# Optimization experiments

Measured on AMD Instinct MI355X. Metric: run time of the kernel, lower is better.

The kernel has to match this reference:

```python
import jax, jax.numpy as jnp
import numpy as np

B, N, D_FEAT = 16, 4096, 64
NPOINT, NSAMPLE = 1024, 32
MLP = [64, 64, 128]
IN_CH = 3 + D_FEAT
EPS = 1e-5  # BatchNorm eps (torch default)


def _fps(xyz, npoint):
    # Farthest point sampling; sequential scan over npoint steps (matches torch loop).
    b, n, _ = xyz.shape
    def step(carry, _):
        distance, farthest = carry  # (B,N) running min dist, (B,) current centroid idx
        centroid = jnp.take_along_axis(xyz, farthest[:, None, None], axis=1)  # (B,1,3)
        d = jnp.sum((xyz - centroid) ** 2, -1)  # (B,N)
        distance = jnp.minimum(distance, d)
        nxt = jnp.argmax(distance, -1).astype(jnp.int32)
        return (distance, nxt), farthest
    init = (jnp.full((b, n), jnp.inf, dtype=xyz.dtype),
            jnp.full((b,), n // 2, dtype=jnp.int32))
    _, centroids = jax.lax.scan(step, init, None, length=npoint)
    return centroids.T  # (B, npoint)


def _gather(pts, idx):
    # pts: (B,N,C); idx: (B,...) int -> (B,...,C)
    return jax.vmap(lambda p, i: p[i])(pts, idx)


def setup_inputs() -> dict:
    key = jax.random.key(0)
    ks = jax.random.split(key, 16)
    inp = {
        'xyz': jax.random.normal(ks[0], (B, N, 3), jnp.float32),
        'points': jax.random.normal(ks[1], (B, N, D_FEAT), jnp.float32),
    }
    last = IN_CH
    for li, oc in enumerate(MLP):
        inp[f'W{li}'] = jax.random.normal(ks[2 + li], (oc, last), jnp.float32) * (1.0 / np.sqrt(last))
        inp[f'b{li}'] = jnp.zeros((oc,), jnp.float32)
        inp[f'g{li}'] = jnp.ones((oc,), jnp.float32)
        inp[f'be{li}'] = jnp.zeros((oc,), jnp.float32)
        last = oc
    C = MLP[-1]; R = C // 8
    inp['aW1'] = jax.random.normal(ks[10], (R, C), jnp.float32) * (1.0 / np.sqrt(C))
    inp['aW2'] = jax.random.normal(ks[11], (C, R), jnp.float32) * (1.0 / np.sqrt(R))
    return inp


def reference(xyz, points, W0, b0, g0, be0, W1, b1, g1, be1, W2, b2, g2, be2, aW1, aW2):
    fps_idx = _fps(xyz, NPOINT)                 # (B,S) int32
    new_xyz = _gather(xyz, fps_idx)             # (B,S,3)
    # squared distances (B,S,N) via matmul expansion (as torch square_distance)
    d = (-2.0 * jnp.einsum('bsc,bnc->bsn', new_xyz, xyz)
         + jnp.sum(new_xyz ** 2, -1)[..., None]
         + jnp.sum(xyz ** 2, -1)[:, None, :])
    _, idx = jax.lax.top_k(-d, NSAMPLE)         # (B,S,k) nearest neighbors
    grouped_xyz = _gather(xyz, idx)             # (B,S,k,3)
    rel = grouped_xyz - new_xyz[:, :, None, :]  # relative coords
    feat = _gather(points, idx)                 # (B,S,k,D)
    g = jnp.concatenate([rel, feat], axis=-1)   # (B,S,k,3+D) channels-last
    # 1x1 conv MLP + BatchNorm (training-mode batch stats) + ReLU
    for (W, b, ga, be) in ((W0, b0, g0, be0), (W1, b1, g1, be1), (W2, b2, g2, be2)):
        g = jnp.einsum('bskc,oc->bsko', g, W) + b
        mu = g.mean(axis=(0, 1, 2))
        var = g.var(axis=(0, 1, 2))
        g = ga * (g - mu) * jax.lax.rsqrt(var + EPS) + be
        g = jax.nn.relu(g)
    new_points = g.max(axis=2)                  # max over nsample -> (B,S,C)
    # channel attention on (B,C,S) == reductions over S here
    avg = new_points.mean(axis=1)               # (B,C)
    mx = new_points.max(axis=1)                 # (B,C)
    def fc(v):
        return jnp.einsum('cr,br->bc', aW2, jax.nn.relu(jnp.einsum('rc,bc->br', aW1, v)))
    scale = jax.nn.sigmoid(fc(avg) + fc(mx))    # (B,C)
    new_points = new_points * scale[:, None, :]
    return new_xyz, new_points, fps_idx
```

## Files before the change

kernel.cpp:

```cpp
#include <hip/hip_runtime.h>
#include <hip/hip_bf16.h>

#define BB 16
#define NN 4096
#define SS 1024
#define KS 32
#define DF 64
#define INC 67
#define C1 64
#define C2 64
#define C3 128
#define ROWS (BB*SS*KS)
#define EPSBN 1e-5f
#define F_INF (__builtin_inff())

typedef __bf16 bf16;
typedef __bf16 bfrag __attribute__((ext_vector_type(8)));
typedef float  ffrag __attribute__((ext_vector_type(4)));
typedef float  f2    __attribute__((ext_vector_type(2)));
typedef unsigned long long u64;

#define OUT_NXYZ 0
#define OUT_NP   49152
#define OUT_FPS  2146304

#define OFF_FPS   0u
#define OFF_NXYZ  65536u
#define OFF_IDX   262144u
#define OFF_STATS 2359296u
#define OFF_ASUM  2555904u
#define OFF_AMAX  2621440u
#define OFF_BNC   2686976u
#define OFF_SCALE 2690048u
#define OFF_NP0   2698240u
#define OFF_YMAX  11086848u
#define OFF_H1    19475456u
#define OFF_H2    86584320u
#define ZERO_BYTES (196608u + 65536u + 65536u)

#define DPP_MAX_STEP(k, ctrl, rmask, bc) { \
  int _lo = __builtin_amdgcn_update_dpp(0, (int)(unsigned)(k), (ctrl), (rmask), 0xf, (bc)); \
  int _hi = __builtin_amdgcn_update_dpp(0, (int)((k)>>32),     (ctrl), (rmask), 0xf, (bc)); \
  u64 _k2 = ((u64)(unsigned)_hi << 32) | (unsigned)_lo; \
  if (_k2 > (k)) (k) = _k2; }

#define DPP_FMAX_STEP(v, ctrl, rmask, bc) { \
  int _t = __builtin_amdgcn_update_dpp(0, __float_as_int(v), (ctrl), (rmask), 0xf, (bc)); \
  (v) = fmaxf((v), __uint_as_float((unsigned)_t)); }

__device__ __forceinline__ u64 dpp_wavemax64(u64 k){
  DPP_MAX_STEP(k, 0x111, 0xf, true)
  DPP_MAX_STEP(k, 0x112, 0xf, true)
  DPP_MAX_STEP(k, 0x114, 0xf, true)
  DPP_MAX_STEP(k, 0x118, 0xf, true)
  DPP_MAX_STEP(k, 0x142, 0xa, false)
  DPP_MAX_STEP(k, 0x143, 0xc, false)
  return k;
}

__device__ __forceinline__ u64 readlane64(u64 k, int lane){
  unsigned lo = (unsigned)__builtin_amdgcn_readlane((int)(unsigned)k, lane);
  unsigned hi = (unsigned)__builtin_amdgcn_readlane((int)(k >> 32),   lane);
  return ((u64)hi << 32) | lo;
}

__device__ __forceinline__ u64 umax64(u64 a, u64 b){ return a > b ? a : b; }

__global__ __launch_bounds__(256) void fps_kernel(const float* __restrict__ xyz,
                                                  int* __restrict__ fps_i,
                                                  float* __restrict__ nxyz_ws,
                                                  float* __restrict__ out)
{
  #pragma clang fp contract(off)
  __shared__ __align__(16) float4 lc[NN];
  __shared__ int lfps[SS];
  __shared__ __align__(16) u64 slotk[2][4];
  int b = blockIdx.x, t = threadIdx.x;
  const float* xb = xyz + (size_t)b*NN*3;
  for (int p = t; p < NN; p += 256){
    lc[p] = make_float4(xb[p*3], xb[p*3+1], xb[p*3+2], 0.f);
  }
  __syncthreads();
  f2 px2[8], py2[8], pz2[8], pd2[8];
  int p0 = t*16;
  #pragma unroll
  for (int j=0;j<8;++j){
    float4 a = lc[p0+2*j], c = lc[p0+2*j+1];
    px2[j] = (f2){a.x, c.x}; py2[j] = (f2){a.y, c.y}; pz2[j] = (f2){a.z, c.z};
    pd2[j] = (f2){F_INF, F_INF};
  }
  float cx = lc[NN/2].x, cy = lc[NN/2].y, cz = lc[NN/2].z;
  if (t==0) lfps[0]=NN/2;
  int wv = t >> 6, lane = t & 63;
  for (int it=1; it<SS; ++it){
    f2 c2x = (f2){cx,cx}, c2y = (f2){cy,cy}, c2z = (f2){cz,cz};
    float bvA=-1.f; int biA=p0;
    float bvB=-1.f; int biB=p0+8;
    #pragma unroll
    for (int j=0;j<4;++j){
      f2 dx = px2[j]-c2x, dy = py2[j]-c2y, dz = pz2[j]-c2z;
      f2 d = (dx*dx + dy*dy) + dz*dz;
      f2 nd = (f2){fminf(pd2[j].x, d.x), fminf(pd2[j].y, d.y)};
      pd2[j]=nd;
      if (nd.x > bvA){ bvA=nd.x; biA=p0+2*j; }
      if (nd.y > bvA){ bvA=nd.y; biA=p0+2*j+1; }
    }
    #pragma unroll
    for (int j=4;j<8;++j){
      f2 dx = px2[j]-c2x, dy = py2[j]-c2y, dz = pz2[j]-c2z;
      f2 d = (dx*dx + dy*dy) + dz*dz;
      f2 nd = (f2){fminf(pd2[j].x, d.x), fminf(pd2[j].y, d.y)};
      pd2[j]=nd;
      if (nd.x > bvB){ bvB=nd.x; biB=p0+2*j; }
      if (nd.y > bvB){ bvB=nd.y; biB=p0+2*j+1; }
    }
    float bv = bvA; int bi = biA;
    if (bvB > bvA){ bv = bvB; bi = biB; }
    float mv = bv;
    DPP_FMAX_STEP(mv, 0x111, 0xf, true)
    DPP_FMAX_STEP(mv, 0x112, 0xf, true)
    DPP_FMAX_STEP(mv, 0x114, 0xf, true)
    DPP_FMAX_STEP(mv, 0x118, 0xf, true)
    DPP_FMAX_STEP(mv, 0x142, 0xa, false)
    DPP_FMAX_STEP(mv, 0x143, 0xc, false)
    float wmax = __uint_as_float((unsigned)__builtin_amdgcn_readlane(__float_as_int(mv), 63));
    u64 em = __ballot(bv == wmax);
    int wl = (int)__builtin_ctzll(em);
    int wbi = __builtin_amdgcn_readlane(bi, wl);
    int p = it & 1;
    if (lane == 0)
      slotk[p][wv] = ((u64)__float_as_uint(wmax) << 32) | (unsigned)(~wbi);
    __syncthreads();
    ulonglong2 sA = *(const ulonglong2*)&slotk[p][0];
    ulonglong2 sB = *(const ulonglong2*)&slotk[p][2];
    u64 k = umax64(umax64(sA.x, sA.y), umax64(sB.x, sB.y));
    int i = ~(unsigned)k;
    float4 cc = lc[i];
    cx = cc.x; cy = cc.y; cz = cc.z;
    if (t==0) lfps[it]=i;
  }
  __syncthreads();
  for (int s=t; s<SS; s+=256){
    int i = lfps[s];
    fps_i[b*SS+s]=i;
    out[OUT_FPS + b*SS + s] = (float)i;
    float4 cc = lc[i];
    int o3 = (b*SS+s)*3;
    out[OUT_NXYZ+o3]=cc.x; out[OUT_NXYZ+o3+1]=cc.y; out[OUT_NXYZ+o3+2]=cc.z;
    nxyz_ws[o3]=cc.x; nxyz_ws[o3+1]=cc.y; nxyz_ws[o3+2]=cc.z;
  }
}

__global__ __launch_bounds__(64) void knn_kernel(const float* __restrict__ xyz,
                                                 const float* __restrict__ nxyz,
                                                 int* __restrict__ knn)
{
  __shared__ float ld[NN];
  int lane = threadIdx.x;
  int bs = blockIdx.x;
  int b = bs >> 10;
  const float* xb = xyz + (size_t)b*NN*3;
  float sx=nxyz[bs*3], sy=nxyz[bs*3+1], sz=nxyz[bs*3+2];
  float gv[8]; int gi[8];
  float lv = F_INF; int li = 0;
  #pragma unroll
  for (int g=0; g<8; ++g){
    float bgv = F_INF; int bgi = 0;
    #pragma unroll
    for (int jj=0; jj<8; ++jj){
      int p = (g*8+jj)*64 + lane;
      float dx=xb[p*3]-sx, dy=xb[p*3+1]-sy, dz=xb[p*3+2]-sz;
      float d = dx*dx+dy*dy+dz*dz;
      ld[p] = d;
      if (d < bgv){ bgv=d; bgi=p; }
    }
    gv[g]=bgv; gi[g]=bgi;
    if (bgv < lv){ lv=bgv; li=bgi; }
  }
  int kept = 0;
  for (int it=0; it<KS; ++it){
    u64 mk = ~(((u64)__float_as_uint(lv) << 32) | (unsigned)li);
    mk = dpp_wavemax64(mk);
    mk = readlane64(mk, 63);
    int i = (int)(unsigned)(~mk);
    if (lane==it) kept = i;
    if ((i & 63) == lane){
      int j = i >> 6;
      ld[i] = F_INF;
      int g = j >> 3;
      float bgv=F_INF; int bgi=0;
      for (int jj=0;jj<8;++jj){
        int p = (g*8+jj)*64 + lane;
        float d = ld[p];
        if (d<bgv){bgv=d;bgi=p;}
      }
      #pragma unroll
      for (int q=0;q<8;++q){ if (q==g){ gv[q]=bgv; gi[q]=bgi; } }
      lv=F_INF; li=0;
      #pragma unroll
      for (int q=0;q<8;++q){ if (gv[q]<lv){ lv=gv[q]; li=gi[q]; } }
    }
  }
  if (lane < KS) knn[bs*KS + lane] = kept;
}

__global__ __launch_bounds__(256) void conv1_kernel(const float* __restrict__ xyz,
                                                    const float* __restrict__ points,
                                                    const float* __restrict__ W0,
                                                    const float* __restrict__ b0,
                                                    const float* __restrict__ nxyz,
                                                    const int* __restrict__ knn,
                                                    bf16* __restrict__ h1,
                                                    float* __restrict__ stats)
{
  __shared__ __align__(16) bf16 As[64][104];
  __shared__ __align__(16) bf16 Bs[64][104];
  __shared__ float s1[C1], s2[C1];
  int t = threadIdx.x;
  int Rbase = blockIdx.x * 64;
  if (t < C1){ s1[t]=0.f; s2[t]=0.f; }
  {
    int o = t >> 2, q = t & 3;
    const float* wr = W0 + o*INC;
    for (int cc = q*24; cc < q*24+24; ++cc){
      float w;
      if (cc < 64) w = wr[3+cc];
      else if (cc < 67) w = wr[cc-64];
      else w = 0.f;
      Bs[o][cc] = (bf16)w;
    }
  }
  {
    int r = t >> 2, q = t & 3;
    int R = Rbase + r;
    int bs = R >> 5;
    int bIdx = bs >> 10;
    int nI = knn[R];
    const float* pr = points + ((size_t)(bIdx*NN + nI))*DF + q*16;
    float4 f0 = *(const float4*)(pr);
    float4 f1 = *(const float4*)(pr+4);
    float4 f2v = *(const float4*)(pr+8);
    float4 f3 = *(const float4*)(pr+12);
    bf16* ap = &As[r][q*16];
    ap[0]=(bf16)f0.x; ap[1]=(bf16)f0.y; ap[2]=(bf16)f0.z; ap[3]=(bf16)f0.w;
    ap[4]=(bf16)f1.x; ap[5]=(bf16)f1.y; ap[6]=(bf16)f1.z; ap[7]=(bf16)f1.w;
    ap[8]=(bf16)f2v.x; ap[9]=(bf16)f2v.y; ap[10]=(bf16)f2v.z; ap[11]=(bf16)f2v.w;
    ap[12]=(bf16)f3.x; ap[13]=(bf16)f3.y; ap[14]=(bf16)f3.z; ap[15]=(bf16)f3.w;
    if (q==0){
      const float* xr = xyz + ((size_t)(bIdx*NN + nI))*3;
      const float* nr = nxyz + bs*3;
      As[r][64]=(bf16)(xr[0]-nr[0]);
      As[r][65]=(bf16)(xr[1]-nr[1]);
      As[r][66]=(bf16)(xr[2]-nr[2]);
      for (int cc=67; cc<96; ++cc) As[r][cc]=(bf16)0.f;
    }
  }
  __syncthreads();
  int wv = t >> 6, lane = t & 63;
  int row16 = wv * 16;
  int arow = lane & 15, kgrp = lane >> 4;
  ffrag acc[4] = {};
  #pragma unroll
  for (int kc = 0; kc < 3; ++kc){
    bfrag af = *(const bfrag*)&As[row16 + arow][kc*32 + kgrp*8];
    #pragma unroll
    for (int nt = 0; nt < 4; ++nt){
      bfrag bfv = *(const bfrag*)&Bs[nt*16 + arow][kc*32 + kgrp*8];
      acc[nt] = __builtin_amdgcn_mfma_f32_16x16x32_bf16(af, bfv, acc[nt], 0,0,0);
    }
  }
  #pragma unroll
  for (int nt=0; nt<4; ++nt){
    int c = nt*16 + arow;
    float bias = b0[c];
    float ls1=0.f, ls2=0.f;
    #pragma unroll
    for (int r=0;r<4;++r){
      float y = acc[nt][r] + bias;
      int grow = Rbase + row16 + kgrp*4 + r;
      h1[(size_t)grow*C1 + c] = (bf16)y;
      ls1 += y; ls2 += y*y;
    }
    ls1 += __shfl_xor(ls1, 16); ls1 += __shfl_xor(ls1, 32);
    ls2 += __shfl_xor(ls2, 16); ls2 += __shfl_xor(ls2, 32);
    if (kgrp==0){ atomicAdd(&s1[c], ls1); atomicAdd(&s2[c], ls2); }
  }
  __syncthreads();
  if (t < C1){
    float* gp = stats + (blockIdx.x & 63)*256;
    atomicAdd(&gp[t], s1[t]);
    atomicAdd(&gp[128 + t], s2[t]);
  }
}

__global__ __launch_bounds__(256) void conv2_kernel(const bf16* __restrict__ h1,
                                                    const float* __restrict__ W1,
                                                    const float* __restrict__ b1,
                                                    const float* __restrict__ stats0,
                                                    const float* __restrict__ g0,
                                                    const float* __restrict__ be0,
                                                    bf16* __restrict__ h2,
                                                    float* __restrict__ stats)
{
  __shared__ __align__(16) bf16 As[64][72];
  __shared__ __align__(16) bf16 Bs[64][72];
  __shared__ float s1[C2], s2[C2];
  __shared__ float sbA[C2], sbB[C2];
  int t = threadIdx.x;
  int Rbase = blockIdx.x * 64;
  if (t < C2){ s1[t]=0.f; s2[t]=0.f; }
  if (t < C2){
    float a1=0.f, a2=0.f;
    for (int q=0;q<64;++q){ a1 += stats0[q*256+t]; a2 += stats0[q*256+128+t]; }
    float inv = 1.f/(float)ROWS;
    float mu = a1*inv; float var = a2*inv - mu*mu;
    float a = g0[t]*rsqrtf(var + EPSBN);
    sbA[t] = a; sbB[t] = be0[t] - mu*a;
  }
  {
    int o = t >> 2, q = t & 3;
    const float* wr = W1 + o*64 + q*16;
    bf16* bp = &Bs[o][q*16];
    #pragma unroll
    for (int v=0; v<4; ++v){
      float4 f = *(const float4*)(wr + v*4);
      bp[v*4+0]=(bf16)f.x; bp[v*4+1]=(bf16)f.y; bp[v*4+2]=(bf16)f.z; bp[v*4+3]=(bf16)f.w;
    }
  }
  __syncthreads();
  {
    int r = t >> 2, q = t & 3;
    int R = Rbase + r;
    const bf16* hr = h1 + (size_t)R*64 + q*16;
    bfrag h0 = *(const bfrag*)hr;
    bfrag h1v = *(const bfrag*)(hr+8);
    #pragma unroll
    for (int j=0;j<8;++j){
      int c=q*16+j;
      As[r][c] = (bf16)fmaxf(fmaf(sbA[c], (float)h0[j], sbB[c]), 0.f);
    }
    #pragma unroll
    for (int j=0;j<8;++j){
      int c=q*16+8+j;
      As[r][c] = (bf16)fmaxf(fmaf(sbA[c], (float)h1v[j], sbB[c]), 0.f);
    }
  }
  __syncthreads();
  int wv = t >> 6, lane = t & 63;
  int row16 = wv * 16;
  int arow = lane & 15, kgrp = lane >> 4;
  ffrag acc[4] = {};
  #pragma unroll
  for (int kc = 0; kc < 2; ++kc){
    bfrag af = *(const bfrag*)&As[row16 + arow][kc*32 + kgrp*8];
    #pragma unroll
    for (int nt = 0; nt < 4; ++nt){
      bfrag bfv = *(const bfrag*)&Bs[nt*16 + arow][kc*32 + kgrp*8];
      acc[nt] = __builtin_amdgcn_mfma_f32_16x16x32_bf16(af, bfv, acc[nt], 0,0,0);
    }
  }
  #pragma unroll
  for (int nt=0; nt<4; ++nt){
    int c = nt*16 + arow;
    float bias = b1[c];
    float ls1=0.f, ls2=0.f;
    #pragma unroll
    for (int r=0;r<4;++r){
      float y = acc[nt][r] + bias;
      int grow = Rbase + row16 + kgrp*4 + r;
      h2[(size_t)grow*C2 + c] = (bf16)y;
      ls1 += y; ls2 += y*y;
    }
    ls1 += __shfl_xor(ls1, 16); ls1 += __shfl_xor(ls1, 32);
    ls2 += __shfl_xor(ls2, 16); ls2 += __shfl_xor(ls2, 32);
    if (kgrp==0){ atomicAdd(&s1[c], ls1); atomicAdd(&s2[c], ls2); }
  }
  __syncthreads();
  if (t < C2){
    float* gp = stats + (blockIdx.x & 63)*256;
    atomicAdd(&gp[t], s1[t]);
    atomicAdd(&gp[128 + t], s2[t]);
  }
}

__global__ __launch_bounds__(256) void conv3_kernel(const bf16* __restrict__ h2,
                                                    const float* __restrict__ W2,
                                                    const float* __restrict__ b2,
                                                    const float* __restrict__ stats1,
                                                    const float* __restrict__ g1,
                                                    const float* __restrict__ be1,
                                                    float* __restrict__ ymax,
                                                    float* __restrict__ stats)
{
  __shared__ __align__(16) bf16 As[64][72];
  __shared__ __align__(16) bf16 Bs[128][72];
  __shared__ float s1[C3], s2[C3];
  __shared__ float wmax[4][C3];
  __shared__ float sbA[C2], sbB[C2];
  int t = threadIdx.x;
  int Rbase = blockIdx.x * 64;
  if (t < C3){ s1[t]=0.f; s2[t]=0.f; }
  if (t < C2){
    float a1=0.f, a2=0.f;
    for (int q=0;q<64;++q){ a1 += stats1[q*256+t]; a2 += stats1[q*256+128+t]; }
    float inv = 1.f/(float)ROWS;
    float mu = a1*inv; float var = a2*inv - mu*mu;
    float a = g1[t]*rsqrtf(var + EPSBN);
    sbA[t] = a; sbB[t] = be1[t] - mu*a;
  }
  {
    int o = t >> 1, q = t & 1;
    const float* wr = W2 + o*64 + q*32;
    bf16* bp = &Bs[o][q*32];
    #pragma unroll
    for (int v=0; v<8; ++v){
      float4 f = *(const float4*)(wr + v*4);
      bp[v*4+0]=(bf16)f.x; bp[v*4+1]=(bf16)f.y; bp[v*4+2]=(bf16)f.z; bp[v*4+3]=(bf16)f.w;
    }
  }
  __syncthreads();
  {
    int r = t >> 2, q = t & 3;
    int R = Rbase + r;
    const bf16* hr = h2 + (size_t)R*64 + q*16;
    bfrag h0 = *(const bfrag*)hr;
    bfrag h1v = *(const bfrag*)(hr+8);
    #pragma unroll
    for (int j=0;j<8;++j){
      int c=q*16+j;
      As[r][c] = (bf16)fmaxf(fmaf(sbA[c], (float)h0[j], sbB[c]), 0.f);
    }
    #pragma unroll
    for (int j=0;j<8;++j){
      int c=q*16+8+j;
      As[r][c] = (bf16)fmaxf(fmaf(sbA[c], (float)h1v[j], sbB[c]), 0.f);
    }
  }
  __syncthreads();
  int wv = t >> 6, lane = t & 63;
  int row16 = wv * 16;
  int arow = lane & 15, kgrp = lane >> 4;
  ffrag acc[8] = {};
  #pragma unroll
  for (int kc = 0; kc < 2; ++kc){
    bfrag af = *(const bfrag*)&As[row16 + arow][kc*32 + kgrp*8];
    #pragma unroll
    for (int nt = 0; nt < 8; ++nt){
      bfrag bfv = *(const bfrag*)&Bs[nt*16 + arow][kc*32 + kgrp*8];
      acc[nt] = __builtin_amdgcn_mfma_f32_16x16x32_bf16(af, bfv, acc[nt], 0,0,0);
    }
  }
  #pragma unroll
  for (int nt=0; nt<8; ++nt){
    int c = nt*16 + arow;
    float bias = b2[c];
    float ls1=0.f, ls2=0.f, mm=-F_INF;
    #pragma unroll
    for (int r=0;r<4;++r){
      float y = acc[nt][r] + bias;
      ls1 += y; ls2 += y*y; mm = fmaxf(mm, y);
    }
    ls1 += __shfl_xor(ls1, 16); ls1 += __shfl_xor(ls1, 32);
    ls2 += __shfl_xor(ls2, 16); ls2 += __shfl_xor(ls2, 32);
    mm = fmaxf(mm, __shfl_xor(mm, 16)); mm = fmaxf(mm, __shfl_xor(mm, 32));
    if (kgrp==0){ atomicAdd(&s1[c], ls1); atomicAdd(&s2[c], ls2); wmax[wv][c]=mm; }
  }
  __syncthreads();
  {
    int half = t >> 7;
    int c = t & 127;
    float m = fmaxf(wmax[half*2][c], wmax[half*2+1][c]);
    ymax[(size_t)(blockIdx.x*2 + half)*C3 + c] = m;
  }
  if (t < C3){
    float* gp = stats + (blockIdx.x & 63)*256;
    atomicAdd(&gp[t], s1[t]);
    atomicAdd(&gp[128 + t], s2[t]);
  }
}

__global__ __launch_bounds__(256) void attreduce_kernel(const float* __restrict__ ymax,
                                                        const float* __restrict__ stats2,
                                                        const float* __restrict__ g2,
                                                        const float* __restrict__ be2,
                                                        float* __restrict__ np0,
                                                        float* __restrict__ asum,
                                                        unsigned* __restrict__ amax)
{
  __shared__ float rs[256], rm[256];
  __shared__ float sbA[C3], sbB[C3];
  int t = threadIdx.x;
  if (t < C3){
    float a1=0.f, a2=0.f;
    for (int q=0;q<64;++q){ a1 += stats2[q*256+t]; a2 += stats2[q*256+128+t]; }
    float inv = 1.f/(float)ROWS;
    float mu = a1*inv; float var = a2*inv - mu*mu;
    float a = g2[t]*rsqrtf(var + EPSBN);
    sbA[t] = a; sbB[t] = be2[t] - mu*a;
  }
  __syncthreads();
  int b = blockIdx.x >> 3, sg = blockIdx.x & 7;
  int c = t & 127, h = t >> 7;
  float a = sbA[c], bb = sbB[c];
  size_t base = ((size_t)(b*1024 + sg*128 + h*64))*128 + c;
  float s = 0.f, m = 0.f;
  #pragma unroll 4
  for (int j=0;j<64;++j){
    float v = fmaxf(fmaf(a, ymax[base + (size_t)j*128], bb), 0.f);
    np0[base + (size_t)j*128] = v;
    s += v; m = fmaxf(m, v);
  }
  rs[t]=s; rm[t]=m;
  __syncthreads();
  if (t < 128){
    float s2 = rs[t] + rs[t+128];
    float m2 = fmaxf(rm[t], rm[t+128]);
    atomicAdd(&asum[b*128+t], s2);
    atomicMax(&amax[b*128+t], __float_as_uint(m2));
  }
}

__global__ __launch_bounds__(256) void attn_kernel(const float* __restrict__ asum,
                                                   const unsigned* __restrict__ amax,
                                                   const float* __restrict__ aW1,
                                                   const float* __restrict__ aW2,
                                                   float* __restrict__ scale)
{
  __shared__ float avg[16][128], mx[16][128], hA[16][16], hM[16][16];
  int t = threadIdx.x;
  for (int i=t; i<2048; i+=256){
    int b=i>>7, c=i&127;
    avg[b][c]=asum[i]*(1.f/1024.f); mx[b][c]=__uint_as_float(amax[i]);
  }
  __syncthreads();
  {
    int b=t>>4, r=t&15;
    float sa=0.f, sm=0.f;
    for (int c=0;c<128;++c){ float w=aW1[r*128+c]; sa+=w*avg[b][c]; sm+=w*mx[b][c]; }
    hA[b][r]=fmaxf(sa,0.f); hM[b][r]=fmaxf(sm,0.f);
  }
  __syncthreads();
  for (int i=t;i<2048;i+=256){
    int b=i>>7,c=i&127;
    float o=0.f;
    for (int r=0;r<16;++r){ o += aW2[c*16+r]*(hA[b][r]+hM[b][r]); }
    scale[i] = 1.f/(1.f+expf(-o));
  }
}

__global__ __launch_bounds__(256) void finout_kernel(const float* __restrict__ np0,
                                                     const float* __restrict__ scale,
                                                     float* __restrict__ out)
{
  int i = blockIdx.x*256 + threadIdx.x;
  int c = i & 127; int b = i >> 17;
  out[OUT_NP + i] = np0[i] * scale[b*128+c];
}

extern "C" void kernel_launch(void* const* d_in, const int* in_sizes, int n_in,
                              void* d_out, int out_size, void* d_ws, size_t ws_size,
                              hipStream_t stream)
{
  const float* xyz    = (const float*)d_in[0];
  const float* points = (const float*)d_in[1];
  const float* W0 = (const float*)d_in[2];
  const float* b0 = (const float*)d_in[3];
  const float* g0 = (const float*)d_in[4];
  const float* be0= (const float*)d_in[5];
  const float* W1 = (const float*)d_in[6];
  const float* b1 = (const float*)d_in[7];
  const float* g1 = (const float*)d_in[8];
  const float* be1= (const float*)d_in[9];
  const float* W2 = (const float*)d_in[10];
  const float* b2 = (const float*)d_in[11];
  const float* g2 = (const float*)d_in[12];
  const float* be2= (const float*)d_in[13];
  const float* aW1= (const float*)d_in[14];
  const float* aW2= (const float*)d_in[15];
  float* out = (float*)d_out;
  char* ws = (char*)d_ws;

  int*      fpsI  = (int*)(ws + OFF_FPS);
  float*    nxyz  = (float*)(ws + OFF_NXYZ);
  int*      knnI  = (int*)(ws + OFF_IDX);
  float*    stats = (float*)(ws + OFF_STATS);
  float*    asum  = (float*)(ws + OFF_ASUM);
  unsigned* amax  = (unsigned*)(ws + OFF_AMAX);
  float*    scl   = (float*)(ws + OFF_SCALE);
  float*    np0   = (float*)(ws + OFF_NP0);
  float*    ymax  = (float*)(ws + OFF_YMAX);
  bf16*     h1    = (bf16*)(ws + OFF_H1);
  bf16*     h2    = (bf16*)(ws + OFF_H2);

  hipMemsetAsync(ws + OFF_STATS, 0, ZERO_BYTES, stream);
  fps_kernel<<<BB, 256, 0, stream>>>(xyz, fpsI, nxyz, out);
  knn_kernel<<<BB*SS, 64, 0, stream>>>(xyz, nxyz, knnI);
  conv1_kernel<<<ROWS/64, 256, 0, stream>>>(xyz, points, W0, b0, nxyz, knnI, h1, stats);
  conv2_kernel<<<ROWS/64, 256, 0, stream>>>(h1, W1, b1, stats, g0, be0, h2, stats + 64*256);
  conv3_kernel<<<ROWS/64, 256, 0, stream>>>(h2, W2, b2, stats + 64*256, g1, be1, ymax, stats + 2*64*256);
  attreduce_kernel<<<BB*8, 256, 0, stream>>>(ymax, stats + 2*64*256, g2, be2, np0, asum, amax);
  attn_kernel<<<1, 256, 0, stream>>>(asum, amax, aW1, aW2, scl);
  finout_kernel<<<(BB*SS*C3)/256, 256, 0, stream>>>(np0, scl, out);
}
```

Baseline: 1.051 ms.

## Double conv row tiles to 128 rows per 512-thread block; merge FPS argmax chains

The three conv kernels now handle 128 rows per block with 512 threads. Each block loads and converts the weight tile once for twice as many rows and issues half as many stats atomics per row. In FPS, the two interleaved argmax chains become one sequential chain over all 8 pairs, which lowers register use but lengthens the dependency chain. Larger blocks also cut the number of blocks and may reduce occupancy. The serial FPS chain could be slower on what is likely the critical path.

```diff
diff --git a/kernel.cpp b/kernel.cpp
--- a/kernel.cpp
+++ b/kernel.cpp
@@ -94,28 +94,16 @@
   int wv = t >> 6, lane = t & 63;
   for (int it=1; it<SS; ++it){
     f2 c2x = (f2){cx,cx}, c2y = (f2){cy,cy}, c2z = (f2){cz,cz};
-    float bvA=-1.f; int biA=p0;
-    float bvB=-1.f; int biB=p0+8;
-    #pragma unroll
-    for (int j=0;j<4;++j){
+    float bv=-1.f; int bi=p0;
+    #pragma unroll
+    for (int j=0;j<8;++j){
       f2 dx = px2[j]-c2x, dy = py2[j]-c2y, dz = pz2[j]-c2z;
       f2 d = (dx*dx + dy*dy) + dz*dz;
       f2 nd = (f2){fminf(pd2[j].x, d.x), fminf(pd2[j].y, d.y)};
       pd2[j]=nd;
-      if (nd.x > bvA){ bvA=nd.x; biA=p0+2*j; }
-      if (nd.y > bvA){ bvA=nd.y; biA=p0+2*j+1; }
-    }
-    #pragma unroll
-    for (int j=4;j<8;++j){
-      f2 dx = px2[j]-c2x, dy = py2[j]-c2y, dz = pz2[j]-c2z;
-      f2 d = (dx*dx + dy*dy) + dz*dz;
-      f2 nd = (f2){fminf(pd2[j].x, d.x), fminf(pd2[j].y, d.y)};
-      pd2[j]=nd;
-      if (nd.x > bvB){ bvB=nd.x; biB=p0+2*j; }
-      if (nd.y > bvB){ bvB=nd.y; biB=p0+2*j+1; }
-    }
-    float bv = bvA; int bi = biA;
-    if (bvB > bvA){ bv = bvB; bi = biB; }
+      if (nd.x > bv){ bv=nd.x; bi=p0+2*j; }
+      if (nd.y > bv){ bv=nd.y; bi=p0+2*j+1; }
+    }
     float mv = bv;
     DPP_FMAX_STEP(mv, 0x111, 0xf, true)
     DPP_FMAX_STEP(mv, 0x112, 0xf, true)
@@ -204,7 +192,7 @@
   if (lane < KS) knn[bs*KS + lane] = kept;
 }
 
-__global__ __launch_bounds__(256) void conv1_kernel(const float* __restrict__ xyz,
+__global__ __launch_bounds__(512) void conv1_kernel(const float* __restrict__ xyz,
                                                     const float* __restrict__ points,
                                                     const float* __restrict__ W0,
                                                     const float* __restrict__ b0,
@@ -213,13 +201,13 @@
                                                     bf16* __restrict__ h1,
                                                     float* __restrict__ stats)
 {
-  __shared__ __align__(16) bf16 As[64][104];
+  __shared__ __align__(16) bf16 As[128][104];
   __shared__ __align__(16) bf16 Bs[64][104];
   __shared__ float s1[C1], s2[C1];
   int t = threadIdx.x;
-  int Rbase = blockIdx.x * 64;
+  int Rbase = blockIdx.x * 128;
   if (t < C1){ s1[t]=0.f; s2[t]=0.f; }
-  {
+  if (t < 256){
     int o = t >> 2, q = t & 3;
     const float* wr = W0 + o*INC;
     for (int cc = q*24; cc < q*24+24; ++cc){
@@ -293,7 +281,7 @@
   }
 }
 
-__global__ __launch_bounds__(256) void conv2_kernel(const bf16* __restrict__ h1,
+__global__ __launch_bounds__(512) void conv2_kernel(const bf16* __restrict__ h1,
                                                     const float* __restrict__ W1,
                                                     const float* __restrict__ b1,
                                                     const float* __restrict__ stats0,
@@ -302,12 +290,12 @@
                                                     bf16* __restrict__ h2,
                                                     float* __restrict__ stats)
 {
-  __shared__ __align__(16) bf16 As[64][72];
+  __shared__ __align__(16) bf16 As[128][72];
   __shared__ __align__(16) bf16 Bs[64][72];
   __shared__ float s1[C2], s2[C2];
   __shared__ float sbA[C2], sbB[C2];
   int t = threadIdx.x;
-  int Rbase = blockIdx.x * 64;
+  int Rbase = blockIdx.x * 128;
   if (t < C2){ s1[t]=0.f; s2[t]=0.f; }
   if (t < C2){
     float a1=0.f, a2=0.f;
@@ -317,7 +305,7 @@
     float a = g0[t]*rsqrtf(var + EPSBN);
     sbA[t] = a; sbB[t] = be0[t] - mu*a;
   }
-  {
+  if (t < 256){
     int o = t >> 2, q = t & 3;
     const float* wr = W1 + o*64 + q*16;
     bf16* bp = &Bs[o][q*16];
@@ -383,7 +371,7 @@
   }
 }
 
-__global__ __launch_bounds__(256) void conv3_kernel(const bf16* __restrict__ h2,
+__global__ __launch_bounds__(512) void conv3_kernel(const bf16* __restrict__ h2,
                                                     const float* __restrict__ W2,
                                                     const float* __restrict__ b2,
                                                     const float* __restrict__ stats1,
@@ -392,13 +380,13 @@
                                                     float* __restrict__ ymax,
                                                     float* __restrict__ stats)
 {
-  __shared__ __align__(16) bf16 As[64][72];
+  __shared__ __align__(16) bf16 As[128][72];
   __shared__ __align__(16) bf16 Bs[128][72];
   __shared__ float s1[C3], s2[C3];
-  __shared__ float wmax[4][C3];
+  __shared__ float wmax[8][C3];
   __shared__ float sbA[C2], sbB[C2];
   int t = threadIdx.x;
-  int Rbase = blockIdx.x * 64;
+  int Rbase = blockIdx.x * 128;
   if (t < C3){ s1[t]=0.f; s2[t]=0.f; }
   if (t < C2){
     float a1=0.f, a2=0.f;
@@ -408,7 +396,7 @@
     float a = g1[t]*rsqrtf(var + EPSBN);
     sbA[t] = a; sbB[t] = be1[t] - mu*a;
   }
-  {
+  if (t < 256){
     int o = t >> 1, q = t & 1;
     const float* wr = W2 + o*64 + q*32;
     bf16* bp = &Bs[o][q*32];
@@ -467,10 +455,10 @@
   }
   __syncthreads();
   {
-    int half = t >> 7;
+    int grp = t >> 7;
     int c = t & 127;
-    float m = fmaxf(wmax[half*2][c], wmax[half*2+1][c]);
-    ymax[(size_t)(blockIdx.x*2 + half)*C3 + c] = m;
+    float m = fmaxf(wmax[grp*2][c], wmax[grp*2+1][c]);
+    ymax[(size_t)(blockIdx.x*4 + grp)*C3 + c] = m;
   }
   if (t < C3){
     float* gp = stats + (blockIdx.x & 63)*256;
@@ -595,9 +583,9 @@
   hipMemsetAsync(ws + OFF_STATS, 0, ZERO_BYTES, stream);
   fps_kernel<<<BB, 256, 0, stream>>>(xyz, fpsI, nxyz, out);
   knn_kernel<<<BB*SS, 64, 0, stream>>>(xyz, nxyz, knnI);
-  conv1_kernel<<<ROWS/64, 256, 0, stream>>>(xyz, points, W0, b0, nxyz, knnI, h1, stats);
-  conv2_kernel<<<ROWS/64, 256, 0, stream>>>(h1, W1, b1, stats, g0, be0, h2, stats + 64*256);
-  conv3_kernel<<<ROWS/64, 256, 0, stream>>>(h2, W2, b2, stats + 64*256, g1, be1, ymax, stats + 2*64*256);
+  conv1_kernel<<<ROWS/128, 512, 0, stream>>>(xyz, points, W0, b0, nxyz, knnI, h1, stats);
+  conv2_kernel<<<ROWS/128, 512, 0, stream>>>(h1, W1, b1, stats, g0, be0, h2, stats + 64*256);
+  conv3_kernel<<<ROWS/128, 512, 0, stream>>>(h2, W2, b2, stats + 64*256, g1, be1, ymax, stats + 2*64*256);
   attreduce_kernel<<<BB*8, 256, 0, stream>>>(ymax, stats + 2*64*256, g2, be2, np0, asum, amax);
   attn_kernel<<<1, 256, 0, stream>>>(asum, amax, aW1, aW2, scl);
   finout_kernel<<<(BB*SS*C3)/256, 256, 0, stream>>>(np0, scl, out);
```

Result: faster. 1.024 ms (-2.6%).
